# Kernel tuning notes

Hardware: AMD Instinct MI355X
Metric: run time of the kernel (lower is better)

Reference implementation:

```python
import jax, jax.numpy as jnp
import numpy as np

K = 32
BN_EPS = 1e-5


def _fps(points, n_samples):
    # Sequential farthest point sampling; deterministic start at index 0
    # (torch version uses a random start; math otherwise identical).
    B, N, _ = points.shape

    def step(carry, _):
        dist_min, far = carry                                   # (B,N), (B,)
        c = jnp.take_along_axis(points, far[:, None, None].astype(jnp.int32) * jnp.ones((1, 1, 3), jnp.int32), axis=1)  # (B,1,3)
        d = jnp.sum((points - c) ** 2, axis=2)                  # (B,N)
        dist_min = jnp.minimum(dist_min, d)
        return (dist_min, jnp.argmax(dist_min, axis=1)), far

    init = (jnp.full((B, N), 1e10, points.dtype), jnp.zeros((B,), jnp.int64).astype(jnp.int32))
    _, cent = jax.lax.scan(step, init, None, length=n_samples)  # (n_samples, B)
    return cent.T                                               # (B, n_samples)


def _knn_idx(cntrds, pnts, k):
    # squared euclidean distance (same neighbor ordering as torch.cdist)
    d2 = (jnp.sum(cntrds ** 2, -1)[:, :, None]
          + jnp.sum(pnts ** 2, -1)[:, None, :]
          - 2.0 * jnp.einsum('bsc,bnc->bsn', cntrds, pnts))     # (B,ns,N)
    _, idx = jax.lax.top_k(-d2, k)                              # smallest-k
    return idx                                                  # (B,ns,k)


def _gather(x, idx):
    # x: (B,N,D), idx: (B,...) -> (B,...,D)
    return jax.vmap(lambda a, i: a[i])(x, idx)


def _conv1x1(x, w):
    # x: (B,Cin,ns,k), w: (Cout,Cin)
    return jnp.einsum('oc,bcnk->bonk', w, x)


def _bn_relu(x, g, b):
    # training-mode BatchNorm2d (biased variance over B,ns,k) + ReLU
    mean = jnp.mean(x, axis=(0, 2, 3), keepdims=True)
    var = jnp.var(x, axis=(0, 2, 3), keepdims=True)
    xh = (x - mean) * jax.lax.rsqrt(var + BN_EPS)
    return jax.nn.relu(xh * g[None, :, None, None] + b[None, :, None, None])


def setup_inputs() -> dict:
    key = jax.random.key(0)
    ks = jax.random.split(key, 16)
    B, N = 4, 4096
    s = 0.05
    return {
        'p': jax.random.normal(ks[0], (B, N, 3), jnp.float32),
        'f': jax.random.normal(ks[1], (B, 3, N), jnp.float32),
        'w1': jax.random.normal(ks[2], (256, 6), jnp.float32) * s,
        'w2': jax.random.normal(ks[3], (256, 256), jnp.float32) * s,
        'b2': jax.random.normal(ks[4], (256,), jnp.float32) * s,
        'g2': jnp.ones((256,), jnp.float32),
        'be2': jnp.zeros((256,), jnp.float32),
        'w3': jax.random.normal(ks[5], (512, 512), jnp.float32) * s,
        'g3': jnp.ones((512,), jnp.float32),
        'be3': jnp.zeros((512,), jnp.float32),
        'w4': jax.random.normal(ks[6], (256, 512), jnp.float32) * s,
        'g4': jnp.ones((256,), jnp.float32),
        'be4': jnp.zeros((256,), jnp.float32),
    }


def reference(p, f, w1, w2, b2, g2, be2, w3, g3, be3, w4, g4, be4):
    B, N, _ = p.shape
    ns = N // 4
    idx_c = _fps(p, ns)                                   # (B,ns)
    cntrd = _gather(p, idx_c)                             # (B,ns,3)
    feats = jnp.transpose(f, (0, 2, 1))                   # (B,N,3)
    knn = _knn_idx(cntrd, p, K)                           # (B,ns,K)
    dp = _gather(p, knn)                                  # (B,ns,K,3)
    fj = _gather(feats, knn)                              # (B,ns,K,3)
    x = jnp.transpose(jnp.concatenate([dp, fj], -1), (0, 3, 1, 2))  # (B,6,ns,K)
    # conv1: 6->256 (no bias), 256->256 (bias) + BN + ReLU
    x = _conv1x1(x, w1)
    x = _conv1x1(x, w2) + b2[None, :, None, None]
    x = _bn_relu(x, g2, be2)                              # (B,256,ns,K)
    xm = jnp.max(x, axis=-1, keepdims=True)
    x = jnp.concatenate([jnp.broadcast_to(xm, x.shape), x], axis=1)  # (B,512,ns,K)
    # conv2: 512->512 BN ReLU, 512->256 BN ReLU
    x = _bn_relu(_conv1x1(x, w3), g3, be3)
    x = _bn_relu(_conv1x1(x, w4), g4, be4)
    out_feat = jnp.max(x, axis=-1)                        # (B,256,ns)
    return cntrd, out_feat
```

## Files before the change

### kernel.cpp

```cpp
#include <hip/hip_runtime.h>
#include <hip/hip_bf16.h>

#define B_ 4
#define N_ 4096
#define NS_ 1024
#define KNN_ 32
#define NPOS_ 131072
#define BN_EPS_ 1e-5f

using bf16 = __hip_bfloat16;
typedef unsigned short us;
typedef __attribute__((ext_vector_type(8))) short short8;
typedef __attribute__((ext_vector_type(4))) float f32x4;
typedef unsigned long long ull;

__device__ __forceinline__ float bf2f(bf16 h){ return __bfloat162float(h); }
__device__ __forceinline__ us f2bfbits(float x){
    bf16 h = __float2bfloat16(x);
    return *reinterpret_cast<us*>(&h);
}
__device__ __forceinline__ float bits2f(us u){
    unsigned v = ((unsigned)u)<<16; return __uint_as_float(v);
}
__device__ __forceinline__ void unpack8(uint4 v, float* f){
    f[0]=__uint_as_float((v.x&0xFFFFu)<<16); f[1]=__uint_as_float(v.x&0xFFFF0000u);
    f[2]=__uint_as_float((v.y&0xFFFFu)<<16); f[3]=__uint_as_float(v.y&0xFFFF0000u);
    f[4]=__uint_as_float((v.z&0xFFFFu)<<16); f[5]=__uint_as_float(v.z&0xFFFF0000u);
    f[6]=__uint_as_float((v.w&0xFFFFu)<<16); f[7]=__uint_as_float(v.w&0xFFFF0000u);
}
__device__ __forceinline__ uint4 pack8(const float* f){
    uint4 v;
    v.x = (unsigned)f2bfbits(f[0]) | ((unsigned)f2bfbits(f[1])<<16);
    v.y = (unsigned)f2bfbits(f[2]) | ((unsigned)f2bfbits(f[3])<<16);
    v.z = (unsigned)f2bfbits(f[4]) | ((unsigned)f2bfbits(f[5])<<16);
    v.w = (unsigned)f2bfbits(f[6]) | ((unsigned)f2bfbits(f[7])<<16);
    return v;
}
__device__ __forceinline__ unsigned fmono(float v){
    unsigned u = __float_as_uint(v);
    return (u & 0x80000000u) ? ~u : (u | 0x80000000u);
}

template<int CTRL, int ROWM>
__device__ __forceinline__ float dppmaxf(float x){
    int xi = __float_as_int(x);
    int yi = __builtin_amdgcn_update_dpp(xi, xi, CTRL, ROWM, 0xF, false);
    return fmaxf(x, __int_as_float(yi));
}
template<int CTRL, int ROWM>
__device__ __forceinline__ float dppminf(float x){
    int xi = __float_as_int(x);
    int yi = __builtin_amdgcn_update_dpp(xi, xi, CTRL, ROWM, 0xF, false);
    return fminf(x, __int_as_float(yi));
}
__device__ __forceinline__ float wave_max_f32(float x){
    x = dppmaxf<0x111,0xF>(x);
    x = dppmaxf<0x112,0xF>(x);
    x = dppmaxf<0x114,0xF>(x);
    x = dppmaxf<0x118,0xF>(x);
    x = dppmaxf<0x142,0xA>(x);
    x = dppmaxf<0x143,0xC>(x);
    return __int_as_float(__builtin_amdgcn_readlane(__float_as_int(x), 63));
}
__device__ __forceinline__ float wave_min_f32(float x){
    x = dppminf<0x111,0xF>(x);
    x = dppminf<0x112,0xF>(x);
    x = dppminf<0x114,0xF>(x);
    x = dppminf<0x118,0xF>(x);
    x = dppminf<0x142,0xA>(x);
    x = dppminf<0x143,0xC>(x);
    return __int_as_float(__builtin_amdgcn_readlane(__float_as_int(x), 63));
}
__device__ __forceinline__ float rowsum16(float x){
    x += __int_as_float(__builtin_amdgcn_update_dpp(0, __float_as_int(x), 0x111, 0xF, 0xF, true));
    x += __int_as_float(__builtin_amdgcn_update_dpp(0, __float_as_int(x), 0x112, 0xF, 0xF, true));
    x += __int_as_float(__builtin_amdgcn_update_dpp(0, __float_as_int(x), 0x114, 0xF, 0xF, true));
    x += __int_as_float(__builtin_amdgcn_update_dpp(0, __float_as_int(x), 0x118, 0xF, 0xF, true));
    return x;
}
__device__ __forceinline__ float max16(const float* v){
    float a = fmaxf(fmaxf(fmaxf(v[0],v[1]),v[2]),v[3]);
    float b = fmaxf(fmaxf(fmaxf(v[4],v[5]),v[6]),v[7]);
    float c = fmaxf(fmaxf(fmaxf(v[8],v[9]),v[10]),v[11]);
    float d = fmaxf(fmaxf(fmaxf(v[12],v[13]),v[14]),v[15]);
    return fmaxf(fmaxf(a,b), fmaxf(c,d));
}
__device__ __forceinline__ float min16(const float* v){
    float a = fminf(fminf(fminf(v[0],v[1]),v[2]),v[3]);
    float b = fminf(fminf(fminf(v[4],v[5]),v[6]),v[7]);
    float c = fminf(fminf(fminf(v[8],v[9]),v[10]),v[11]);
    float d = fminf(fminf(fminf(v[12],v[13]),v[14]),v[15]);
    return fminf(fminf(a,b), fminf(c,d));
}

#define NSLOT 64

__global__ __launch_bounds__(256) void bn_coef(const float* __restrict__ part,
                                               const float* __restrict__ g,
                                               const float* __restrict__ be,
                                               int chbase, int C,
                                               float2* __restrict__ ab){
    int c = blockIdx.x*256 + threadIdx.x;
    if (c < C){
        const float* ps = part + (size_t)(chbase+c)*2*NSLOT;
        float s = 0.f, q = 0.f;
        #pragma unroll 8
        for (int i=0;i<NSLOT;i++){ s += ps[i]; q += ps[NSLOT+i]; }
        const float inv = 1.0f/(float)NPOS_;
        float mean = s*inv;
        float var  = q*inv - mean*mean;
        float a = g[c]*rsqrtf(var + BN_EPS_);
        ab[c] = make_float2(a, be[c] - mean*a);
    }
}

__global__ __launch_bounds__(256) void fps_plus(const float* __restrict__ p,
                                                int* __restrict__ idxc,
                                                float* __restrict__ cntrd,
                                                float* __restrict__ part,
                                                const float* __restrict__ w1,
                                                const float* __restrict__ w2,
                                                float* __restrict__ W26,
                                                const float* __restrict__ w3,
                                                us* __restrict__ whi3, us* __restrict__ wlo3,
                                                const float* __restrict__ w4,
                                                us* __restrict__ whi4, us* __restrict__ wlo4){
    __shared__ float4 pxyz[N_];
    __shared__ ull warr[2][4];
    const int bid = blockIdx.x;
    const int t = threadIdx.x;
    if (bid >= 4){
        if (bid < 516){
            part[(bid-4)*256 + t] = 0.0f;
        } else if (bid == 516){
            float acc[6] = {0,0,0,0,0,0};
            for (int k=0;k<256;k++){
                float w2v = w2[t*256+k];
                #pragma unroll
                for (int j=0;j<6;j++) acc[j] = fmaf(w2v, w1[k*6+j], acc[j]);
            }
            #pragma unroll
            for (int j=0;j<6;j++) W26[j*256+t] = acc[j];
        } else if (bid < 1541){
            int i = (bid-517)*256 + t;
            float x = w3[i];
            us h = f2bfbits(x);
            whi3[i] = h;
            wlo3[i] = f2bfbits(__fsub_rn(x, bits2f(h)));
        } else {
            int i = (bid-1541)*256 + t;
            float x = w4[i];
            us h = f2bfbits(x);
            whi4[i] = h;
            wlo4[i] = f2bfbits(__fsub_rn(x, bits2f(h)));
        }
        return;
    }
    const int b = bid;
    const int lane = t & 63;
    const int wave = t >> 6;
    const float* pb = p + (size_t)b*N_*3;
    float rx[16], ry[16], rz[16], dist[16];
    #pragma unroll
    for (int j=0;j<16;j++){
        int i = t*16+j;
        float x = pb[i*3+0];
        float y = pb[i*3+1];
        float z = pb[i*3+2];
        rx[j]=x; ry[j]=y; rz[j]=z;
        pxyz[i] = make_float4(x,y,z,0.f);
        dist[j]=1e10f;
    }
    __syncthreads();
    int cur = 0;
    float4 c = pxyz[0];
    if (t==0){
        idxc[b*NS_] = 0;
        cntrd[(size_t)(b*NS_)*3+0] = c.x;
        cntrd[(size_t)(b*NS_)*3+1] = c.y;
        cntrd[(size_t)(b*NS_)*3+2] = c.z;
    }
    for (int s=1; s<NS_; s++){
        #pragma unroll
        for (int j=0;j<16;j++){
            float dx = __fsub_rn(rx[j],c.x);
            float dy = __fsub_rn(ry[j],c.y);
            float dz = __fsub_rn(rz[j],c.z);
            float d  = __fadd_rn(__fadd_rn(__fmul_rn(dx,dx),__fmul_rn(dy,dy)),__fmul_rn(dz,dz));
            dist[j] = fminf(dist[j], d);
        }
        float lmax = max16(dist);
        float wmax = wave_max_f32(lmax);
        unsigned msk = 0;
        #pragma unroll
        for (int j=0;j<16;j++) msk |= (dist[j]==wmax) ? (1u<<j) : 0u;
        ull ball = __ballot(msk != 0);
        int srclane = (int)__builtin_ctzll(ball);
        unsigned lmsk = (unsigned)__builtin_amdgcn_readlane((int)msk, srclane);
        int widx = (wave*64 + srclane)*16 + (int)__builtin_ctz(lmsk);
        if (lane==0)
            warr[s&1][wave] = ((ull)__float_as_uint(wmax)<<32) | (0xFFFFFFFFu - (unsigned)widx);
        __syncthreads();
        ull g0 = warr[s&1][0], g1 = warr[s&1][1], g2 = warr[s&1][2], g3 = warr[s&1][3];
        ull ga = g0 > g1 ? g0 : g1;
        ull gb = g2 > g3 ? g2 : g3;
        ull g  = ga > gb ? ga : gb;
        cur = (int)(0xFFFFFFFFu - (unsigned)(g & 0xFFFFFFFFull));
        c = pxyz[cur];
        if (t==0){
            idxc[b*NS_+s] = cur;
            cntrd[(size_t)(b*NS_+s)*3+0] = c.x;
            cntrd[(size_t)(b*NS_+s)*3+1] = c.y;
            cntrd[(size_t)(b*NS_+s)*3+2] = c.z;
        }
    }
}

__global__ __launch_bounds__(256) void convknn_kernel(const float* __restrict__ p,
                                                      const float* __restrict__ f,
                                                      const int* __restrict__ idxc,
                                                      const float* __restrict__ W26,
                                                      const float* __restrict__ b2,
                                                      bf16* __restrict__ z2,
                                                      float* __restrict__ part){
    __shared__ ull warr[2][4];
    __shared__ int knnS[32];
    __shared__ float Ws[6][256];
    __shared__ float xs[6][32];
    const int bid = blockIdx.x;
    const int b = bid >> 10;
    const int t = threadIdx.x;
    const int lane = t & 63;
    const int wave = t >> 6;
    const float* pb = p + (size_t)b*N_*3;
    #pragma unroll
    for (int r=0;r<6;r++) Ws[r][t] = W26[r*256+t];
    const int ci = idxc[bid];
    float cx = pb[ci*3+0];
    float cy = pb[ci*3+1];
    float cz = pb[ci*3+2];
    float c2 = __fadd_rn(__fadd_rn(__fmul_rn(cx,cx),__fmul_rn(cy,cy)),__fmul_rn(cz,cz));
    float d2[16];
    #pragma unroll
    for (int j=0;j<16;j++){
        int i = t*16+j;
        float x = pb[i*3+0];
        float y = pb[i*3+1];
        float z = pb[i*3+2];
        float p2 = __fadd_rn(__fadd_rn(__fmul_rn(x,x),__fmul_rn(y,y)),__fmul_rn(z,z));
        float dot= __fadd_rn(__fadd_rn(__fmul_rn(cx,x),__fmul_rn(cy,y)),__fmul_rn(cz,z));
        d2[j] = __fsub_rn(__fadd_rn(c2,p2), __fmul_rn(2.0f,dot));
    }
    for (int it=0; it<KNN_; it++){
        float lmin = min16(d2);
        float wmin = wave_min_f32(lmin);
        unsigned msk = 0;
        #pragma unroll
        for (int j=0;j<16;j++) msk |= (d2[j]==wmin) ? (1u<<j) : 0u;
        ull ball = __ballot(msk != 0);
        int srclane = (int)__builtin_ctzll(ball);
        unsigned lmsk = (unsigned)__builtin_amdgcn_readlane((int)msk, srclane);
        int widx = (wave*64 + srclane)*16 + (int)__builtin_ctz(lmsk);
        if (lane==0)
            warr[it&1][wave] = ((ull)fmono(wmin)<<32) | (unsigned)widx;
        __syncthreads();
        ull g0 = warr[it&1][0], g1 = warr[it&1][1], g2 = warr[it&1][2], g3 = warr[it&1][3];
        ull ga = g0 < g1 ? g0 : g1;
        ull gb = g2 < g3 ? g2 : g3;
        ull g  = ga < gb ? ga : gb;
        int idx = (int)(g & 0xFFFFFFFFull);
        if ((idx>>4)==t) d2[idx & 15] = INFINITY;
        if (t==0) knnS[it] = idx;
    }
    __syncthreads();
    if (t < 32){
        int i = knnS[t];
        const float* fb = f + (size_t)b*3*N_;
        xs[0][t] = pb[i*3+0];
        xs[1][t] = pb[i*3+1];
        xs[2][t] = pb[i*3+2];
        xs[3][t] = fb[0*N_+i];
        xs[4][t] = fb[1*N_+i];
        xs[5][t] = fb[2*N_+i];
    }
    __syncthreads();
    float w0=Ws[0][t], w1v=Ws[1][t], w2v=Ws[2][t], w3v=Ws[3][t], w4v=Ws[4][t], w5v=Ws[5][t];
    float bias = b2[t];
    bf16* zrow = z2 + (size_t)t*NPOS_ + (size_t)bid*KNN_;
    float ssum = 0.f, sq = 0.f;
    for (int k0=0;k0<32;k0+=8){
        float y[8];
        #pragma unroll
        for (int u=0;u<8;u++){
            int k = k0+u;
            float acc = bias;
            acc = fmaf(w0, xs[0][k], acc);
            acc = fmaf(w1v,xs[1][k], acc);
            acc = fmaf(w2v,xs[2][k], acc);
            acc = fmaf(w3v,xs[3][k], acc);
            acc = fmaf(w4v,xs[4][k], acc);
            acc = fmaf(w5v,xs[5][k], acc);
            float vr = bits2f(f2bfbits(acc));
            ssum += vr; sq = fmaf(vr, vr, sq);
            y[u] = acc;
        }
        *reinterpret_cast<uint4*>(zrow + k0) = pack8(y);
    }
    const int slot = bid & (NSLOT-1);
    atomicAdd(&part[(size_t)(t*2+0)*NSLOT + slot], ssum);
    atomicAdd(&part[(size_t)(t*2+1)*NSLOT + slot], sq);
}

__global__ __launch_bounds__(256) void xm_kernel(const bf16* __restrict__ z2raw,
                                                 const float2* __restrict__ ab,
                                                 bf16* __restrict__ xm){
    int gid = blockIdx.x*256 + threadIdx.x;
    int c = gid >> 12;
    int bs = gid & 4095;
    float2 s = ab[c];
    const uint4* xp = reinterpret_cast<const uint4*>(z2raw + (size_t)c*NPOS_ + (size_t)bs*KNN_);
    float m = 0.0f;
    #pragma unroll
    for (int r=0;r<4;r++){
        uint4 v = xp[r];
        float fv[8]; unpack8(v, fv);
        #pragma unroll
        for (int u=0;u<8;u++) m = fmaxf(m, fmaf(fv[u], s.x, s.y));
    }
    xm[(size_t)c*4096 + bs] = __float2bfloat16(m);
}

__global__ __launch_bounds__(256) void gemm128(const float* __restrict__ A, int lda, int aoff,
                                               const bf16* __restrict__ B,
                                               int M, int N, int K,
                                               float* __restrict__ Cf){
    __shared__ float As[16][128];
    __shared__ float Bs[16][128];
    const int tid = threadIdx.x;
    const int tx = tid & 15, ty = tid >> 4;
    const int m0 = blockIdx.y*128, n0 = blockIdx.x*128;
    float acc[8][8];
    #pragma unroll
    for (int i=0;i<8;i++)
        #pragma unroll
        for (int j=0;j<8;j++) acc[i][j]=0.f;
    const int arow = tid >> 1, akg = tid & 1;
    const int bkk = tid >> 4, bng = tid & 15;
    for (int k0=0;k0<K;k0+=16){
        const float* aptr = A + (size_t)(m0+arow)*lda + aoff + k0 + akg*8;
        float4 a0 = *reinterpret_cast<const float4*>(aptr);
        float4 a1 = *reinterpret_cast<const float4*>(aptr+4);
        As[akg*8+0][arow]=a0.x; As[akg*8+1][arow]=a0.y;
        As[akg*8+2][arow]=a0.z; As[akg*8+3][arow]=a0.w;
        As[akg*8+4][arow]=a1.x; As[akg*8+5][arow]=a1.y;
        As[akg*8+6][arow]=a1.z; As[akg*8+7][arow]=a1.w;
        uint4 bv = *reinterpret_cast<const uint4*>(B + (size_t)(k0+bkk)*N + n0 + bng*8);
        float bf[8]; unpack8(bv, bf);
        *reinterpret_cast<float4*>(&Bs[bkk][bng*8+0]) = make_float4(bf[0],bf[1],bf[2],bf[3]);
        *reinterpret_cast<float4*>(&Bs[bkk][bng*8+4]) = make_float4(bf[4],bf[5],bf[6],bf[7]);
        __syncthreads();
        #pragma unroll
        for (int kk=0;kk<16;kk++){
            float a[8], b[8];
            *reinterpret_cast<float4*>(&a[0]) = *reinterpret_cast<float4*>(&As[kk][ty*8+0]);
            *reinterpret_cast<float4*>(&a[4]) = *reinterpret_cast<float4*>(&As[kk][ty*8+4]);
            *reinterpret_cast<float4*>(&b[0]) = *reinterpret_cast<float4*>(&Bs[kk][tx*8+0]);
            *reinterpret_cast<float4*>(&b[4]) = *reinterpret_cast<float4*>(&Bs[kk][tx*8+4]);
            #pragma unroll
            for (int i=0;i<8;i++)
                #pragma unroll
                for (int j=0;j<8;j++)
                    acc[i][j] = fmaf(a[i], b[j], acc[i][j]);
        }
        __syncthreads();
    }
    const int n = n0 + tx*8;
    #pragma unroll
    for (int i=0;i<8;i++){
        int m = m0 + ty*8 + i;
        *reinterpret_cast<float4*>(Cf + (size_t)m*N + n + 0) = make_float4(acc[i][0],acc[i][1],acc[i][2],acc[i][3]);
        *reinterpret_cast<float4*>(Cf + (size_t)m*N + n + 4) = make_float4(acc[i][4],acc[i][5],acc[i][6],acc[i][7]);
    }
}

#define LDK 40
__global__ __launch_bounds__(256) void gemm_mfma(const us* __restrict__ Whi,
                                                 const us* __restrict__ Wlo,
                                                 int ldw, int aoff,
                                                 const bf16* __restrict__ act, int K,
                                                 const float2* __restrict__ ab,
                                                 bf16* __restrict__ out,
                                                 const float* __restrict__ t3,
                                                 float* __restrict__ part, int chbase){
    __shared__ __align__(16) us AsH[128*LDK];
    __shared__ __align__(16) us AsL[128*LDK];
    __shared__ __align__(16) us Bs [128*LDK];
    __shared__ float t3s[128][4];
    const us* actu = reinterpret_cast<const us*>(act);
    const int t = threadIdx.x;
    const int m0 = blockIdx.x*128, n0 = blockIdx.y*128;
    const int wave = t>>6, lane = t&63;
    const int wm = wave>>1, wn = wave&1;
    const int q = lane>>4, col = lane&15;

    if (t3 && t < 128){
        const float* src = t3 + (size_t)(m0+t)*4096 + (n0>>5);
        t3s[t][0]=src[0]; t3s[t][1]=src[1]; t3s[t][2]=src[2]; t3s[t][3]=src[3];
    }

    f32x4 acc[4][4];
    #pragma unroll
    for (int i=0;i<4;i++)
        #pragma unroll
        for (int j=0;j<4;j++) acc[i][j] = (f32x4){0.f,0.f,0.f,0.f};

    const int ar = t>>1, ah = t&1;
    const int bn = t&127, bh = t>>7;

    for (int k0=0;k0<K;k0+=32){
        const us* sh = Whi + (size_t)(m0+ar)*ldw + aoff + k0 + ah*16;
        const us* sl = Wlo + (size_t)(m0+ar)*ldw + aoff + k0 + ah*16;
        uint4 h0 = *reinterpret_cast<const uint4*>(sh);
        uint4 h1 = *reinterpret_cast<const uint4*>(sh+8);
        uint4 l0 = *reinterpret_cast<const uint4*>(sl);
        uint4 l1 = *reinterpret_cast<const uint4*>(sl+8);
        *reinterpret_cast<uint4*>(&AsH[ar*LDK + ah*16 + 0]) = h0;
        *reinterpret_cast<uint4*>(&AsH[ar*LDK + ah*16 + 8]) = h1;
        *reinterpret_cast<uint4*>(&AsL[ar*LDK + ah*16 + 0]) = l0;
        *reinterpret_cast<uint4*>(&AsL[ar*LDK + ah*16 + 8]) = l1;
        us bvals[16];
        #pragma unroll
        for (int j=0;j<16;j++){
            int k = k0 + bh*16 + j;
            float x = bits2f(actu[(size_t)k*NPOS_ + n0 + bn]);
            float2 s = ab[k];
            bvals[j] = f2bfbits(fmaxf(fmaf(x, s.x, s.y), 0.0f));
        }
        *reinterpret_cast<uint4*>(&Bs[bn*LDK + bh*16 + 0]) = *reinterpret_cast<uint4*>(&bvals[0]);
        *reinterpret_cast<uint4*>(&Bs[bn*LDK + bh*16 + 8]) = *reinterpret_cast<uint4*>(&bvals[8]);
        __syncthreads();
        short8 bf[4], afh[4], afl[4];
        #pragma unroll
        for (int tn=0;tn<4;tn++)
            bf[tn] = *reinterpret_cast<const short8*>(&Bs[(wn*64+tn*16+col)*LDK + q*8]);
        #pragma unroll
        for (int tm=0;tm<4;tm++){
            afh[tm] = *reinterpret_cast<const short8*>(&AsH[(wm*64+tm*16+col)*LDK + q*8]);
            afl[tm] = *reinterpret_cast<const short8*>(&AsL[(wm*64+tm*16+col)*LDK + q*8]);
        }
        #pragma unroll
        for (int tm=0;tm<4;tm++)
            #pragma unroll
            for (int tn=0;tn<4;tn++){
                acc[tm][tn] = __builtin_amdgcn_mfma_f32_16x16x32_bf16(afh[tm], bf[tn], acc[tm][tn], 0, 0, 0);
                acc[tm][tn] = __builtin_amdgcn_mfma_f32_16x16x32_bf16(afl[tm], bf[tn], acc[tm][tn], 0, 0, 0);
            }
        __syncthreads();
    }
    const int slot = (int)(blockIdx.y & (NSLOT-1));
    #pragma unroll
    for (int tm=0;tm<4;tm++){
        #pragma unroll
        for (int r=0;r<4;r++){
            int m_l = wm*64 + tm*16 + q*4 + r;
            float srow = 0.f, qrow = 0.f;
            #pragma unroll
            for (int tn=0;tn<4;tn++){
                int n_l = wn*64 + tn*16 + col;
                float vv = acc[tm][tn][r];
                if (t3) vv += t3s[m_l][n_l>>5];
                us hb = f2bfbits(vv);
                reinterpret_cast<us*>(out)[(size_t)(m0+m_l)*NPOS_ + n0 + n_l] = hb;
                float vr = bits2f(hb);
                srow += vr; qrow = fmaf(vr, vr, qrow);
            }
            srow = rowsum16(srow);
            qrow = rowsum16(qrow);
            if (col == 15){
                atomicAdd(&part[(size_t)((chbase + m0 + m_l)*2+0)*NSLOT + slot], srow);
                atomicAdd(&part[(size_t)((chbase + m0 + m_l)*2+1)*NSLOT + slot], qrow);
            }
        }
    }
}

__global__ __launch_bounds__(256) void final_kernel(const bf16* __restrict__ z4,
                                                    const float2* __restrict__ ab,
                                                    float* __restrict__ out){
    int gid = blockIdx.x*256 + threadIdx.x;
    int s = gid & 1023;
    int c = (gid >> 10) & 255;
    int b = gid >> 18;
    int bsi = b*NS_ + s;
    float2 sc = ab[c];
    const uint4* zp = reinterpret_cast<const uint4*>(z4 + (size_t)c*NPOS_ + (size_t)bsi*KNN_);
    float m = 0.0f;
    #pragma unroll
    for (int r=0;r<4;r++){
        uint4 v = zp[r];
        float fv[8]; unpack8(v, fv);
        #pragma unroll
        for (int u=0;u<8;u++) m = fmaxf(m, fmaf(fv[u], sc.x, sc.y));
    }
    out[(size_t)(b*256 + c)*NS_ + s] = m;
}

extern "C" void kernel_launch(void* const* d_in, const int* in_sizes, int n_in,
                              void* d_out, int out_size, void* d_ws, size_t ws_size,
                              hipStream_t stream) {
    const float* p   = (const float*)d_in[0];
    const float* f   = (const float*)d_in[1];
    const float* w1  = (const float*)d_in[2];
    const float* w2  = (const float*)d_in[3];
    const float* b2  = (const float*)d_in[4];
    const float* g2  = (const float*)d_in[5];
    const float* be2 = (const float*)d_in[6];
    const float* w3  = (const float*)d_in[7];
    const float* g3  = (const float*)d_in[8];
    const float* be3 = (const float*)d_in[9];
    const float* w4  = (const float*)d_in[10];
    const float* g4  = (const float*)d_in[11];
    const float* be4 = (const float*)d_in[12];

    char* ws = (char*)d_ws;
    int*    idxc = (int*)(ws + 0);
    float*  W26  = (float*)(ws + 540672);
    float2* ab2  = (float2*)(ws + 555008);
    float2* ab3  = (float2*)(ws + 557056);
    us* whi3 = (us*)(ws + 561152);
    us* wlo3 = (us*)(ws + 1085440);
    us* whi4 = (us*)(ws + 1609728);
    us* wlo4 = (us*)(ws + 1871872);
    float*  t3   = (float*)(ws + 2134016);
    bf16*   z2   = (bf16*)(ws + 10522624);
    bf16*   xm   = (bf16*)(ws + 77631488);
    bf16*   z3   = (bf16*)(ws + 79728640);
    float*  part = (float*)(ws + 213946368);
    float2* ab4  = (float2*)(ws + 214470656);
    bf16*   z4   = z2;

    float* out_cntrd = (float*)d_out;
    float* out_feat  = (float*)d_out + (size_t)B_*NS_*3;

    fps_plus<<<2053, 256, 0, stream>>>(p, idxc, out_cntrd, part,
                                       w1, w2, W26, w3, whi3, wlo3, w4, whi4, wlo4);
    convknn_kernel<<<B_*NS_, 256, 0, stream>>>(p, f, idxc, W26, b2, z2, part);
    bn_coef<<<1, 256, 0, stream>>>(part, g2, be2, 0, 256, ab2);
    xm_kernel<<<4096, 256, 0, stream>>>(z2, ab2, xm);
    gemm128<<<dim3(32,4), 256, 0, stream>>>(w3, 512, 0, xm, 512, 4096, 256, t3);
    gemm_mfma<<<dim3(4,1024), 256, 0, stream>>>(whi3, wlo3, 512, 256, z2, 256, ab2, z3, t3, part, 256);
    bn_coef<<<2, 256, 0, stream>>>(part, g3, be3, 256, 512, ab3);
    gemm_mfma<<<dim3(2,1024), 256, 0, stream>>>(whi4, wlo4, 512, 0, z3, 512, ab3, z4, nullptr, part, 768);
    bn_coef<<<1, 256, 0, stream>>>(part, g4, be4, 768, 256, ab4);
    final_kernel<<<4096, 256, 0, stream>>>(z4, ab4, out_feat);
}
```

Before: 1.253 ms.

## Fuse FPS and kNN/conv into one persistent kernel with progress flags

Merges the sequential farthest-point-sampling kernel and the kNN+first-conv kernel into a single launch. kNN blocks spin on per-sample progress flags that the FPS blocks publish with atomics, so neighbour search and the first conv overlap with the long serial FPS loop instead of waiting for it to finish. Zeroing of the partial sums and flags moves to a memset. The risk is spinning blocks occupying CUs, and a possible deadlock if FPS blocks are not scheduled first. FPS blocks have the lowest ids, which makes that unlikely.

```diff
diff --git a/kernel.cpp b/kernel.cpp
--- a/kernel.cpp
+++ b/kernel.cpp
@@ -114,128 +114,131 @@
     }
 }
 
-__global__ __launch_bounds__(256) void fps_plus(const float* __restrict__ p,
-                                                int* __restrict__ idxc,
-                                                float* __restrict__ cntrd,
-                                                float* __restrict__ part,
-                                                const float* __restrict__ w1,
-                                                const float* __restrict__ w2,
-                                                float* __restrict__ W26,
-                                                const float* __restrict__ w3,
-                                                us* __restrict__ whi3, us* __restrict__ wlo3,
-                                                const float* __restrict__ w4,
-                                                us* __restrict__ whi4, us* __restrict__ wlo4){
+__global__ __launch_bounds__(256) void mega_kernel(const float* __restrict__ p,
+                                                   const float* __restrict__ f,
+                                                   float* __restrict__ cntrd,
+                                                   float* __restrict__ part,
+                                                   int* __restrict__ prog,
+                                                   int* __restrict__ w26flag,
+                                                   const float* __restrict__ w1,
+                                                   const float* __restrict__ w2,
+                                                   float* __restrict__ W26,
+                                                   const float* __restrict__ b2,
+                                                   const float* __restrict__ w3,
+                                                   us* __restrict__ whi3, us* __restrict__ wlo3,
+                                                   const float* __restrict__ w4,
+                                                   us* __restrict__ whi4, us* __restrict__ wlo4,
+                                                   bf16* __restrict__ z2){
     __shared__ float4 pxyz[N_];
-    __shared__ ull warr[2][4];
-    const int bid = blockIdx.x;
-    const int t = threadIdx.x;
-    if (bid >= 4){
-        if (bid < 516){
-            part[(bid-4)*256 + t] = 0.0f;
-        } else if (bid == 516){
-            float acc[6] = {0,0,0,0,0,0};
-            for (int k=0;k<256;k++){
-                float w2v = w2[t*256+k];
-                #pragma unroll
-                for (int j=0;j<6;j++) acc[j] = fmaf(w2v, w1[k*6+j], acc[j]);
-            }
-            #pragma unroll
-            for (int j=0;j<6;j++) W26[j*256+t] = acc[j];
-        } else if (bid < 1541){
-            int i = (bid-517)*256 + t;
-            float x = w3[i];
-            us h = f2bfbits(x);
-            whi3[i] = h;
-            wlo3[i] = f2bfbits(__fsub_rn(x, bits2f(h)));
-        } else {
-            int i = (bid-1541)*256 + t;
-            float x = w4[i];
-            us h = f2bfbits(x);
-            whi4[i] = h;
-            wlo4[i] = f2bfbits(__fsub_rn(x, bits2f(h)));
-        }
-        return;
-    }
-    const int b = bid;
-    const int lane = t & 63;
-    const int wave = t >> 6;
-    const float* pb = p + (size_t)b*N_*3;
-    float rx[16], ry[16], rz[16], dist[16];
-    #pragma unroll
-    for (int j=0;j<16;j++){
-        int i = t*16+j;
-        float x = pb[i*3+0];
-        float y = pb[i*3+1];
-        float z = pb[i*3+2];
-        rx[j]=x; ry[j]=y; rz[j]=z;
-        pxyz[i] = make_float4(x,y,z,0.f);
-        dist[j]=1e10f;
-    }
-    __syncthreads();
-    int cur = 0;
-    float4 c = pxyz[0];
-    if (t==0){
-        idxc[b*NS_] = 0;
-        cntrd[(size_t)(b*NS_)*3+0] = c.x;
-        cntrd[(size_t)(b*NS_)*3+1] = c.y;
-        cntrd[(size_t)(b*NS_)*3+2] = c.z;
-    }
-    for (int s=1; s<NS_; s++){
-        #pragma unroll
-        for (int j=0;j<16;j++){
-            float dx = __fsub_rn(rx[j],c.x);
-            float dy = __fsub_rn(ry[j],c.y);
-            float dz = __fsub_rn(rz[j],c.z);
-            float d  = __fadd_rn(__fadd_rn(__fmul_rn(dx,dx),__fmul_rn(dy,dy)),__fmul_rn(dz,dz));
-            dist[j] = fminf(dist[j], d);
-        }
-        float lmax = max16(dist);
-        float wmax = wave_max_f32(lmax);
-        unsigned msk = 0;
-        #pragma unroll
-        for (int j=0;j<16;j++) msk |= (dist[j]==wmax) ? (1u<<j) : 0u;
-        ull ball = __ballot(msk != 0);
-        int srclane = (int)__builtin_ctzll(ball);
-        unsigned lmsk = (unsigned)__builtin_amdgcn_readlane((int)msk, srclane);
-        int widx = (wave*64 + srclane)*16 + (int)__builtin_ctz(lmsk);
-        if (lane==0)
-            warr[s&1][wave] = ((ull)__float_as_uint(wmax)<<32) | (0xFFFFFFFFu - (unsigned)widx);
-        __syncthreads();
-        ull g0 = warr[s&1][0], g1 = warr[s&1][1], g2 = warr[s&1][2], g3 = warr[s&1][3];
-        ull ga = g0 > g1 ? g0 : g1;
-        ull gb = g2 > g3 ? g2 : g3;
-        ull g  = ga > gb ? ga : gb;
-        cur = (int)(0xFFFFFFFFu - (unsigned)(g & 0xFFFFFFFFull));
-        c = pxyz[cur];
-        if (t==0){
-            idxc[b*NS_+s] = cur;
-            cntrd[(size_t)(b*NS_+s)*3+0] = c.x;
-            cntrd[(size_t)(b*NS_+s)*3+1] = c.y;
-            cntrd[(size_t)(b*NS_+s)*3+2] = c.z;
-        }
-    }
-}
-
-__global__ __launch_bounds__(256) void convknn_kernel(const float* __restrict__ p,
-                                                      const float* __restrict__ f,
-                                                      const int* __restrict__ idxc,
-                                                      const float* __restrict__ W26,
-                                                      const float* __restrict__ b2,
-                                                      bf16* __restrict__ z2,
-                                                      float* __restrict__ part){
     __shared__ ull warr[2][4];
     __shared__ int knnS[32];
     __shared__ float Ws[6][256];
     __shared__ float xs[6][32];
+    __shared__ int ciS;
     const int bid = blockIdx.x;
-    const int b = bid >> 10;
     const int t = threadIdx.x;
     const int lane = t & 63;
     const int wave = t >> 6;
+
+    if (bid < 4){
+        const int b = bid;
+        const float* pb = p + (size_t)b*N_*3;
+        float rx[16], ry[16], rz[16], dist[16];
+        #pragma unroll
+        for (int j=0;j<16;j++){
+            int i = t*16+j;
+            float x = pb[i*3+0];
+            float y = pb[i*3+1];
+            float z = pb[i*3+2];
+            rx[j]=x; ry[j]=y; rz[j]=z;
+            pxyz[i] = make_float4(x,y,z,0.f);
+            dist[j]=1e10f;
+        }
+        __syncthreads();
+        float4 c = pxyz[0];
+        if (t==0){
+            atomicExch(&prog[b*NS_], 1);
+            cntrd[(size_t)(b*NS_)*3+0] = c.x;
+            cntrd[(size_t)(b*NS_)*3+1] = c.y;
+            cntrd[(size_t)(b*NS_)*3+2] = c.z;
+        }
+        for (int s=1; s<NS_; s++){
+            #pragma unroll
+            for (int j=0;j<16;j++){
+                float dx = __fsub_rn(rx[j],c.x);
+                float dy = __fsub_rn(ry[j],c.y);
+                float dz = __fsub_rn(rz[j],c.z);
+                float d  = __fadd_rn(__fadd_rn(__fmul_rn(dx,dx),__fmul_rn(dy,dy)),__fmul_rn(dz,dz));
+                dist[j] = fminf(dist[j], d);
+            }
+            float lmax = max16(dist);
+            float wmax = wave_max_f32(lmax);
+            unsigned msk = 0;
+            #pragma unroll
+            for (int j=0;j<16;j++) msk |= (dist[j]==wmax) ? (1u<<j) : 0u;
+            ull ball = __ballot(msk != 0);
+            int srclane = (int)__builtin_ctzll(ball);
+            unsigned lmsk = (unsigned)__builtin_amdgcn_readlane((int)msk, srclane);
+            int widx = (wave*64 + srclane)*16 + (int)__builtin_ctz(lmsk);
+            if (lane==0)
+                warr[s&1][wave] = ((ull)__float_as_uint(wmax)<<32) | (0xFFFFFFFFu - (unsigned)widx);
+            __syncthreads();
+            ull g0 = warr[s&1][0], g1 = warr[s&1][1], g2 = warr[s&1][2], g3 = warr[s&1][3];
+            ull ga = g0 > g1 ? g0 : g1;
+            ull gb = g2 > g3 ? g2 : g3;
+            ull g  = ga > gb ? ga : gb;
+            int cur = (int)(0xFFFFFFFFu - (unsigned)(g & 0xFFFFFFFFull));
+            c = pxyz[cur];
+            if (t==0){
+                atomicExch(&prog[b*NS_+s], cur+1);
+                cntrd[(size_t)(b*NS_+s)*3+0] = c.x;
+                cntrd[(size_t)(b*NS_+s)*3+1] = c.y;
+                cntrd[(size_t)(b*NS_+s)*3+2] = c.z;
+            }
+        }
+        return;
+    }
+    if (bid == 4){
+        float acc[6] = {0,0,0,0,0,0};
+        for (int k=0;k<256;k++){
+            float w2v = w2[t*256+k];
+            #pragma unroll
+            for (int j=0;j<6;j++) acc[j] = fmaf(w2v, w1[k*6+j], acc[j]);
+        }
+        #pragma unroll
+        for (int j=0;j<6;j++) W26[j*256+t] = acc[j];
+        __syncthreads();
+        if (t==0){ __threadfence(); atomicExch(w26flag, 1); }
+        return;
+    }
+    if (bid < 1029){
+        int i = (bid-5)*256 + t;
+        float x = w3[i];
+        us h = f2bfbits(x);
+        whi3[i] = h;
+        wlo3[i] = f2bfbits(__fsub_rn(x, bits2f(h)));
+        return;
+    }
+    if (bid < 1541){
+        int i = (bid-1029)*256 + t;
+        float x = w4[i];
+        us h = f2bfbits(x);
+        whi4[i] = h;
+        wlo4[i] = f2bfbits(__fsub_rn(x, bits2f(h)));
+        return;
+    }
+    const int wid = bid - 1541;
+    const int b = wid & 3;
+    const int si = wid >> 2;
+    const int sidx = b*NS_ + si;
     const float* pb = p + (size_t)b*N_*3;
-    #pragma unroll
-    for (int r=0;r<6;r++) Ws[r][t] = W26[r*256+t];
-    const int ci = idxc[bid];
+    if (t == 0){
+        int v;
+        while ((v = atomicAdd(&prog[sidx], 0)) == 0) {}
+        ciS = v - 1;
+    }
+    __syncthreads();
+    const int ci = ciS;
     float cx = pb[ci*3+0];
     float cy = pb[ci*3+1];
     float cz = pb[ci*3+2];
@@ -272,7 +275,10 @@
         if ((idx>>4)==t) d2[idx & 15] = INFINITY;
         if (t==0) knnS[it] = idx;
     }
+    if (t == 0){ while (atomicAdd(w26flag, 0) == 0) {} __threadfence(); }
     __syncthreads();
+    #pragma unroll
+    for (int r=0;r<6;r++) Ws[r][t] = W26[r*256+t];
     if (t < 32){
         int i = knnS[t];
         const float* fb = f + (size_t)b*3*N_;
@@ -286,7 +292,7 @@
     __syncthreads();
     float w0=Ws[0][t], w1v=Ws[1][t], w2v=Ws[2][t], w3v=Ws[3][t], w4v=Ws[4][t], w5v=Ws[5][t];
     float bias = b2[t];
-    bf16* zrow = z2 + (size_t)t*NPOS_ + (size_t)bid*KNN_;
+    bf16* zrow = z2 + (size_t)t*NPOS_ + (size_t)sidx*KNN_;
     float ssum = 0.f, sq = 0.f;
     for (int k0=0;k0<32;k0+=8){
         float y[8];
@@ -306,7 +312,7 @@
         }
         *reinterpret_cast<uint4*>(zrow + k0) = pack8(y);
     }
-    const int slot = bid & (NSLOT-1);
+    const int slot = wid & (NSLOT-1);
     atomicAdd(&part[(size_t)(t*2+0)*NSLOT + slot], ssum);
     atomicAdd(&part[(size_t)(t*2+1)*NSLOT + slot], sq);
 }
@@ -523,7 +529,6 @@
     const float* be4 = (const float*)d_in[12];
 
     char* ws = (char*)d_ws;
-    int*    idxc = (int*)(ws + 0);
     float*  W26  = (float*)(ws + 540672);
     float2* ab2  = (float2*)(ws + 555008);
     float2* ab3  = (float2*)(ws + 557056);
@@ -536,15 +541,18 @@
     bf16*   xm   = (bf16*)(ws + 77631488);
     bf16*   z3   = (bf16*)(ws + 79728640);
     float*  part = (float*)(ws + 213946368);
-    float2* ab4  = (float2*)(ws + 214470656);
+    int*    prog = (int*)(ws + 214470656);
+    int*    w26flag = (int*)(ws + 214487040);
+    float2* ab4  = (float2*)(ws + 214487104);
     bf16*   z4   = z2;
 
     float* out_cntrd = (float*)d_out;
     float* out_feat  = (float*)d_out + (size_t)B_*NS_*3;
 
-    fps_plus<<<2053, 256, 0, stream>>>(p, idxc, out_cntrd, part,
-                                       w1, w2, W26, w3, whi3, wlo3, w4, whi4, wlo4);
-    convknn_kernel<<<B_*NS_, 256, 0, stream>>>(p, f, idxc, W26, b2, z2, part);
+    hipMemsetAsync(ws + 213946368, 0, 540676, stream);
+    mega_kernel<<<5637, 256, 0, stream>>>(p, f, out_cntrd, part, prog, w26flag,
+                                          w1, w2, W26, b2,
+                                          w3, whi3, wlo3, w4, whi4, wlo4, z2);
     bn_coef<<<1, 256, 0, stream>>>(part, g2, be2, 0, 256, ab2);
     xm_kernel<<<4096, 256, 0, stream>>>(z2, ab2, xm);
     gemm128<<<dim3(32,4), 256, 0, stream>>>(w3, 512, 0, xm, 512, 4096, 256, t3);
```

Measured after the change: 1.136 ms. -9.4%, faster.
